# Performance work log

Hardware: AMD Instinct MI355X
Metric: run time of the kernel (lower is better)

## Reference

```python
import jax, jax.numpy as jnp
import numpy as np

KMAX, PH, PW, HID = 15, 16, 16, 64

def _rope(x):
    # x: (B, H, T, D); standard rotary, half-split rotation, base 10000
    D = x.shape[-1]; T = x.shape[-2]; half = D // 2
    inv_freq = 1.0 / (10000.0 ** (jnp.arange(half, dtype=jnp.float32) / half))
    ang = jnp.arange(T, dtype=jnp.float32)[:, None] * inv_freq[None, :]  # (T, half)
    cos, sin = jnp.cos(ang), jnp.sin(ang)
    x1, x2 = x[..., :half], x[..., half:]
    return jnp.concatenate([x1 * cos - x2 * sin, x1 * sin + x2 * cos], axis=-1)

def _normalize(v):
    return v / jnp.maximum(jnp.linalg.norm(v, axis=-1, keepdims=True), 1e-12)

def setup_inputs() -> dict:
    key = jax.random.key(0)
    ks = jax.random.split(key, 10)
    B, T, D = 2, 2048, 1024
    rel_in = KMAX + 2  # K gram cols + feat_a + delta
    s = D ** -0.5
    f32 = jnp.float32
    return {
        "x": jax.random.normal(ks[0], (B, T, D), f32),
        "Wi": jax.random.normal(ks[1], (D, D), f32) * s,
        "Wp": jax.random.normal(ks[2], (D, D), f32) * s,
        "palette": jax.random.normal(ks[3], (D, PH, PW), f32) * s,
        "W1": jax.random.normal(ks[4], (rel_in, HID), f32) * rel_in ** -0.5,
        "b1": jnp.zeros((HID,), f32),
        "W2": jax.random.normal(ks[5], (HID, HID), f32) * HID ** -0.5,
        "b2": jnp.zeros((HID,), f32),
        "Wc": jax.random.normal(ks[6], (HID, 2), f32) * HID ** -0.5,
        "bc": jnp.zeros((2,), f32),
        "Wm": jax.random.normal(ks[7], (HID, 1), f32) * HID ** -0.5,
        "bm": jnp.zeros((1,), f32),
        "Wo": jax.random.normal(ks[8], (1, D, D), f32) * s,
    }

def reference(x, Wi, Wp, palette, W1, b1, W2, b2, Wc, bc, Wm, bm, Wo):
    B, T, D = x.shape
    K = KMAX
    scale = D ** -0.5
    I = _rope((x @ Wi)[:, None])        # (B,1,T,D)
    P = _rope((x @ Wp)[:, None])[:, 0]  # (B,T,D)
    logits = jnp.einsum('bhtd,bsd->bhts', I, P) * scale
    causal = jnp.tril(jnp.ones((T, T), dtype=bool))
    logits = jnp.where(causal[None, None], logits, -jnp.inf)
    topk_val, topk_idx = jax.lax.top_k(logits, K)  # (B,1,T,K); T>=K so no pad branch
    keep = jnp.isfinite(topk_val)
    keep_f = keep.astype(x.dtype)
    # diagonal is always kept -> torch 'all_bad' fallback never fires
    P_sel = jax.vmap(lambda p, idx: p[idx])(P, topk_idx)      # (B,1,T,K,D)
    P_sel_norm = _normalize(P_sel) * keep_f[..., None]
    I_norm = _normalize(I)[:, :, :, None, :]                  # (B,1,T,1,D)
    feat_a = jnp.clip(jnp.sum(I_norm * P_sel_norm, -1), -1.0, 1.0) * keep_f
    G = jnp.clip(jnp.einsum('bhtkd,bhtjd->bhtkj', P_sel_norm, P_sel_norm), -1.0, 1.0)
    G = G * keep_f[..., :, None] * keep_f[..., None, :]
    t_range = jnp.arange(T)[None, None, :, None]
    delta = jnp.maximum((t_range - topk_idx).astype(x.dtype), 0.0) / float(max(1, T)) * keep_f
    rel = jnp.concatenate([G, feat_a[..., None], delta[..., None]], axis=-1)  # (B,1,T,K,K+2)
    h = jax.nn.gelu(rel @ W1 + b1, approximate=False)
    h = jax.nn.gelu(h @ W2 + b2, approximate=False)
    z = jnp.tanh(h @ Wc + bc)                                  # (B,1,T,K,2)
    mix = jnp.where(keep, (h @ Wm + bm)[..., 0], -jnp.inf)
    w = jnp.nan_to_num(jax.nn.softmax(mix, axis=-1))           # (B,1,T,K)
    # bilinear grid_sample: align_corners=True, padding_mode='border'
    gx, gy = z[:, 0, :, :, 0], z[:, 0, :, :, 1]                # (B,T,K)
    fx = jnp.clip((gx + 1.0) * 0.5 * (PW - 1), 0.0, PW - 1)
    fy = jnp.clip((gy + 1.0) * 0.5 * (PH - 1), 0.0, PH - 1)
    x0 = jnp.floor(fx).astype(jnp.int32); x1 = jnp.minimum(x0 + 1, PW - 1)
    y0 = jnp.floor(fy).astype(jnp.int32); y1 = jnp.minimum(y0 + 1, PH - 1)
    wx = fx - x0.astype(fx.dtype); wy = fy - y0.astype(fy.dtype)
    pal = palette.reshape(D, PH * PW)
    def g(yi, xi):  # -> (B,T,K,D)
        return jnp.moveaxis(pal[:, yi * PW + xi], 0, -1)
    samples = ((1 - wy) * (1 - wx))[..., None] * g(y0, x0) \
            + ((1 - wy) * wx)[..., None] * g(y0, x1) \
            + (wy * (1 - wx))[..., None] * g(y1, x0) \
            + (wy * wx)[..., None] * g(y1, x1)                 # (B,T,K,D)
    V = jnp.einsum('btkd,btk->btd', samples, w[:, 0])
    y = jnp.einsum('btd,dm->btm', V, Wo[0])  # einsum nrtd,rdm->nrtm then mean over r=1
    return y
```

## Files before the change

kernel.cpp:

```cpp
#include <hip/hip_runtime.h>
#include <math.h>

#define BATCH 2
#define T_LEN 2048
#define D_DIM 1024
#define KSEL  15
#define HIDN  64
#define NCAND 20

typedef short  bf16x8 __attribute__((ext_vector_type(8)));
typedef float  f32x4v __attribute__((ext_vector_type(4)));

__device__ __forceinline__ float geluf(float x) {
  return 0.5f * x * (1.0f + erff(x * 0.70710678118654752440f));
}

__device__ __forceinline__ unsigned short f32_to_bf16_rne(float x) {
  unsigned u = __builtin_bit_cast(unsigned, x);
  unsigned lsb = (u >> 16) & 1u;
  u += 0x7fffu + lsb;
  return (unsigned short)(u >> 16);
}
__device__ __forceinline__ float bf16_to_f32(unsigned short h) {
  unsigned u = ((unsigned)h) << 16;
  return __builtin_bit_cast(float, u);
}

__global__ void __launch_bounds__(256) xsplit3(const float* __restrict__ X,
                                               unsigned short* __restrict__ H,
                                               unsigned short* __restrict__ M,
                                               unsigned short* __restrict__ L)
{
  const size_t i = ((size_t)blockIdx.x * 256 + threadIdx.x) * 4;
  float4 v = *(const float4*)(X + i);
  ushort4 h, m, l;
  float r;
  h.x = f32_to_bf16_rne(v.x); r = v.x - bf16_to_f32(h.x);
  m.x = f32_to_bf16_rne(r);   l.x = f32_to_bf16_rne(r - bf16_to_f32(m.x));
  h.y = f32_to_bf16_rne(v.y); r = v.y - bf16_to_f32(h.y);
  m.y = f32_to_bf16_rne(r);   l.y = f32_to_bf16_rne(r - bf16_to_f32(m.y));
  h.z = f32_to_bf16_rne(v.z); r = v.z - bf16_to_f32(h.z);
  m.z = f32_to_bf16_rne(r);   l.z = f32_to_bf16_rne(r - bf16_to_f32(m.z));
  h.w = f32_to_bf16_rne(v.w); r = v.w - bf16_to_f32(h.w);
  m.w = f32_to_bf16_rne(r);   l.w = f32_to_bf16_rne(r - bf16_to_f32(m.w));
  *(ushort4*)(H + i) = h;
  *(ushort4*)(M + i) = m;
  *(ushort4*)(L + i) = l;
}

__global__ void __launch_bounds__(256) wsplit3T(const float* __restrict__ Wi,
                                                const float* __restrict__ Wp,
                                                unsigned short* __restrict__ WT)
{
  __shared__ float tile[64][65];
  const int k0 = blockIdx.y << 6, n0 = blockIdx.x << 6;
  const int z = blockIdx.z;
  const float* W = z ? Wp : Wi;
  unsigned short* H = WT + (size_t)z * 3 * 1024 * 1024;
  unsigned short* M = H + (size_t)1024 * 1024;
  unsigned short* L = M + (size_t)1024 * 1024;
  const int tid = threadIdx.x;
  for (int idx = tid; idx < 4096; idx += 256) {
    int r = idx >> 6, c = idx & 63;
    tile[r][c] = W[(size_t)(k0 + r) * D_DIM + n0 + c];
  }
  __syncthreads();
  for (int idx = tid; idx < 4096; idx += 256) {
    int n = idx >> 6, k = idx & 63;
    float v = tile[k][n];
    unsigned short h = f32_to_bf16_rne(v);
    float r1 = v - bf16_to_f32(h);
    unsigned short m = f32_to_bf16_rne(r1);
    unsigned short l = f32_to_bf16_rne(r1 - bf16_to_f32(m));
    size_t o = (size_t)(n0 + n) * D_DIM + k0 + k;
    H[o] = h; M[o] = m; L[o] = l;
  }
}

__global__ void __launch_bounds__(256) gemm3bf(
    const unsigned short* __restrict__ Xh, const unsigned short* __restrict__ Xm,
    const unsigned short* __restrict__ Xl, const unsigned short* __restrict__ WT,
    float* __restrict__ C)
{
  const int m0 = blockIdx.y << 6, n0 = blockIdx.x << 6;
  const int z = blockIdx.z;
  const unsigned short* BhT = WT + (size_t)z * 3 * 1024 * 1024;
  const unsigned short* BmT = BhT + (size_t)1024 * 1024;
  const unsigned short* BlT = BmT + (size_t)1024 * 1024;
  C += (size_t)z * 4096 * 1024;
  const int N = D_DIM, K = D_DIM;

  const int tid = threadIdx.x;
  const int w = tid >> 6, lane = tid & 63;
  const int kg = lane >> 4, lm = lane & 15;
  const int am0 = (w & 1) << 5;
  const int bn0 = (w >> 1) << 5;

  __shared__ unsigned short Ah[2][64][40], Am[2][64][40], Al[2][64][40];
  __shared__ unsigned short Bh[2][64][40], Bm[2][64][40], Bl[2][64][40];

  bf16x8 ones;
#pragma unroll
  for (int e = 0; e < 8; ++e) ones[e] = (short)0x3F80;

  for (int idx = tid; idx < 2048; idx += 256) {
    Ah[0][idx >> 5][idx & 31] = f32_to_bf16_rne((float)(idx >> 5));
    Bh[0][idx >> 5][idx & 31] = f32_to_bf16_rne((float)(idx >> 5));
  }
  __syncthreads();
  int mr[4], nc[4];
  {
    bf16x8 pa = *(const bf16x8*)&Ah[0][am0 + lm][kg << 3];
    bf16x8 pb = *(const bf16x8*)&Bh[0][bn0 + lm][kg << 3];
    f32x4v d1 = {0.f, 0.f, 0.f, 0.f}, d2 = {0.f, 0.f, 0.f, 0.f};
    d1 = __builtin_amdgcn_mfma_f32_16x16x32_bf16(pa, ones, d1, 0, 0, 0);
    d2 = __builtin_amdgcn_mfma_f32_16x16x32_bf16(ones, pb, d2, 0, 0, 0);
#pragma unroll
    for (int e = 0; e < 4; ++e) {
      mr[e] = ((int)d1[e]) >> 5;
      nc[e] = ((int)d2[e]) >> 5;
    }
  }
  __syncthreads();

  f32x4v ch[2][2], cm[2][2], cl[2][2];
#pragma unroll
  for (int i = 0; i < 2; ++i)
#pragma unroll
    for (int j = 0; j < 2; ++j) {
      ch[i][j] = (f32x4v){0.f, 0.f, 0.f, 0.f};
      cm[i][j] = (f32x4v){0.f, 0.f, 0.f, 0.f};
      cl[i][j] = (f32x4v){0.f, 0.f, 0.f, 0.f};
    }

  const int ar = tid >> 2, ak8 = (tid & 3) << 3;

  bf16x8 rah, ram, ral, rbh, rbm, rbl;

  {
    size_t ao = (size_t)(m0 + ar) * K + ak8;
    size_t bo = (size_t)(n0 + ar) * K + ak8;
    rah = *(const bf16x8*)(Xh + ao); ram = *(const bf16x8*)(Xm + ao);
    ral = *(const bf16x8*)(Xl + ao);
    rbh = *(const bf16x8*)(BhT + bo); rbm = *(const bf16x8*)(BmT + bo);
    rbl = *(const bf16x8*)(BlT + bo);
  }
  *(bf16x8*)&Ah[0][ar][ak8] = rah;
  *(bf16x8*)&Am[0][ar][ak8] = ram;
  *(bf16x8*)&Al[0][ar][ak8] = ral;
  *(bf16x8*)&Bh[0][ar][ak8] = rbh;
  *(bf16x8*)&Bm[0][ar][ak8] = rbm;
  *(bf16x8*)&Bl[0][ar][ak8] = rbl;
  __syncthreads();

  int buf = 0;
  for (int k0 = 0; k0 < K; k0 += 32) {
    const bool more = (k0 + 32) < K;
    if (more) {
      const int kn = k0 + 32;
      size_t ao = (size_t)(m0 + ar) * K + kn + ak8;
      size_t bo = (size_t)(n0 + ar) * K + kn + ak8;
      rah = *(const bf16x8*)(Xh + ao); ram = *(const bf16x8*)(Xm + ao);
      ral = *(const bf16x8*)(Xl + ao);
      rbh = *(const bf16x8*)(BhT + bo); rbm = *(const bf16x8*)(BmT + bo);
      rbl = *(const bf16x8*)(BlT + bo);
    }
    {
      bf16x8 a_h[2], a_m[2], a_l[2], b_h[2], b_m[2], b_l[2];
#pragma unroll
      for (int i = 0; i < 2; ++i) {
        const int rrow = am0 + (i << 4) + lm;
        a_h[i] = *(const bf16x8*)&Ah[buf][rrow][kg << 3];
        a_m[i] = *(const bf16x8*)&Am[buf][rrow][kg << 3];
        a_l[i] = *(const bf16x8*)&Al[buf][rrow][kg << 3];
        const int nrow = bn0 + (i << 4) + lm;
        b_h[i] = *(const bf16x8*)&Bh[buf][nrow][kg << 3];
        b_m[i] = *(const bf16x8*)&Bm[buf][nrow][kg << 3];
        b_l[i] = *(const bf16x8*)&Bl[buf][nrow][kg << 3];
      }
#pragma unroll
      for (int i = 0; i < 2; ++i)
#pragma unroll
        for (int j = 0; j < 2; ++j) {
          ch[i][j] = __builtin_amdgcn_mfma_f32_16x16x32_bf16(a_h[i], b_h[j], ch[i][j], 0, 0, 0);
          cm[i][j] = __builtin_amdgcn_mfma_f32_16x16x32_bf16(a_h[i], b_m[j], cm[i][j], 0, 0, 0);
          cm[i][j] = __builtin_amdgcn_mfma_f32_16x16x32_bf16(a_m[i], b_h[j], cm[i][j], 0, 0, 0);
          cl[i][j] = __builtin_amdgcn_mfma_f32_16x16x32_bf16(a_h[i], b_l[j], cl[i][j], 0, 0, 0);
          cl[i][j] = __builtin_amdgcn_mfma_f32_16x16x32_bf16(a_m[i], b_m[j], cl[i][j], 0, 0, 0);
          cl[i][j] = __builtin_amdgcn_mfma_f32_16x16x32_bf16(a_l[i], b_h[j], cl[i][j], 0, 0, 0);
        }
    }
    if (more) {
      const int nb = buf ^ 1;
      *(bf16x8*)&Ah[nb][ar][ak8] = rah;
      *(bf16x8*)&Am[nb][ar][ak8] = ram;
      *(bf16x8*)&Al[nb][ar][ak8] = ral;
      *(bf16x8*)&Bh[nb][ar][ak8] = rbh;
      *(bf16x8*)&Bm[nb][ar][ak8] = rbm;
      *(bf16x8*)&Bl[nb][ar][ak8] = rbl;
    }
    __syncthreads();
    buf ^= 1;
  }

#pragma unroll
  for (int i = 0; i < 2; ++i)
#pragma unroll
    for (int j = 0; j < 2; ++j)
#pragma unroll
      for (int e = 0; e < 4; ++e) {
        const int rrow = m0 + mr[e] + (i << 4);
        const int ccol = n0 + nc[e] + (j << 4);
        float v = (ch[i][j][e] + cm[i][j][e]) + cl[i][j][e];
        C[(size_t)rrow * N + ccol] = v;
      }
}

__global__ void __launch_bounds__(256) prep_kernel(float2* __restrict__ tab,
                                                   const float* __restrict__ pal,
                                                   float* __restrict__ palT)
{
  const int b = blockIdx.x;
  if (b < T_LEN) {
    const int t = b;
    for (int j = threadIdx.x; j < 512; j += 256) {
      double e = (double)j * (1.0 / 512.0);
      float pf = (float)pow(10000.0, e);
      float invf = 1.0f / pf;
      float angf = (float)t * invf;
      double s64, c64;
      sincos((double)angf, &s64, &c64);
      tab[(size_t)t * 512 + j] = make_float2((float)c64, (float)s64);
    }
  } else {
    const int bb = b - T_LEN;
    const int c = bb & 255, dg = bb >> 8;
    const int d = dg * 256 + threadIdx.x;
    palT[(size_t)c * D_DIM + d] = pal[(size_t)d * 256 + c];
  }
}

__global__ void __launch_bounds__(256) rope_norm_kernel(
    float* __restrict__ bI, float* __restrict__ bP,
    const float2* __restrict__ tab,
    float* __restrict__ nI, float* __restrict__ nP,
    unsigned short* __restrict__ Ih, unsigned short* __restrict__ Ph)
{
  const int row = blockIdx.x;
  const int t = row & (T_LEN - 1);
  const int tid = threadIdx.x;
  __shared__ double redI[4], redP[4];
  double ssI = 0.0, ssP = 0.0;
  const size_t off = (size_t)row * D_DIM;
  for (int j = tid; j < 512; j += 256) {
    float2 cs = tab[(size_t)t * 512 + j];
    float c = cs.x, s = cs.y;

    float a1 = bI[off + j], a2 = bI[off + 512 + j];
    float o1 = __fsub_rn(__fmul_rn(a1, c), __fmul_rn(a2, s));
    float o2 = __fadd_rn(__fmul_rn(a1, s), __fmul_rn(a2, c));
    bI[off + j] = o1; bI[off + 512 + j] = o2;
    Ih[off + j] = f32_to_bf16_rne(o1); Ih[off + 512 + j] = f32_to_bf16_rne(o2);
    ssI += (double)o1 * o1 + (double)o2 * o2;

    float p1 = bP[off + j], p2 = bP[off + 512 + j];
    float q1 = __fsub_rn(__fmul_rn(p1, c), __fmul_rn(p2, s));
    float q2 = __fadd_rn(__fmul_rn(p1, s), __fmul_rn(p2, c));
    bP[off + j] = q1; bP[off + 512 + j] = q2;
    Ph[off + j] = f32_to_bf16_rne(q1); Ph[off + 512 + j] = f32_to_bf16_rne(q2);
    ssP += (double)q1 * q1 + (double)q2 * q2;
  }
#pragma unroll
  for (int o = 32; o >= 1; o >>= 1) { ssI += __shfl_xor(ssI, o); ssP += __shfl_xor(ssP, o); }
  if ((tid & 63) == 0) { redI[tid >> 6] = ssI; redP[tid >> 6] = ssP; }
  __syncthreads();
  if (tid == 0) {
    nI[row] = fmaxf((float)sqrt(redI[0] + redI[1] + redI[2] + redI[3]), 1e-12f);
    nP[row] = fmaxf((float)sqrt(redP[0] + redP[1] + redP[2] + redP[3]), 1e-12f);
  }
}

__global__ void __launch_bounds__(256) screen_bf16(
    const unsigned short* __restrict__ Ih, const unsigned short* __restrict__ Ph,
    unsigned short* __restrict__ Ssc)
{
  int rem = blockIdx.x, bi = 0;
  while (rem >= (bi >> 1) + 1) { rem -= (bi >> 1) + 1; ++bi; }
  const int m0 = bi << 6, n0 = rem << 7;
  const int z = blockIdx.z;
  const unsigned short* A = Ih + (size_t)z * T_LEN * D_DIM;
  const unsigned short* B = Ph + (size_t)z * T_LEN * D_DIM;
  unsigned short* C = Ssc + (size_t)z * T_LEN * T_LEN;
  const int N = T_LEN, K = D_DIM;

  const int tid = threadIdx.x;
  const int w = tid >> 6, lane = tid & 63;
  const int kg = lane >> 4, lm = lane & 15;
  const int am0 = (w & 1) << 5;
  const int bn0 = (w >> 1) << 6;

  __shared__ unsigned short As_h[2][64][40];
  __shared__ unsigned short Bs_h[2][128][40];

  bf16x8 ones;
#pragma unroll
  for (int e = 0; e < 8; ++e) ones[e] = (short)0x3F80;

  for (int idx = tid; idx < 2048; idx += 256)
    As_h[0][idx >> 5][idx & 31] = f32_to_bf16_rne((float)(idx >> 5));
  for (int idx = tid; idx < 4096; idx += 256)
    Bs_h[0][idx >> 5][idx & 31] = f32_to_bf16_rne((float)(idx >> 5));
  __syncthreads();
  int mr[4], nc[4];
  {
    bf16x8 pa = *(const bf16x8*)&As_h[0][am0 + lm][kg << 3];
    bf16x8 pb = *(const bf16x8*)&Bs_h[0][bn0 + lm][kg << 3];
    f32x4v d1 = {0.f, 0.f, 0.f, 0.f}, d2 = {0.f, 0.f, 0.f, 0.f};
    d1 = __builtin_amdgcn_mfma_f32_16x16x32_bf16(pa, ones, d1, 0, 0, 0);
    d2 = __builtin_amdgcn_mfma_f32_16x16x32_bf16(ones, pb, d2, 0, 0, 0);
#pragma unroll
    for (int e = 0; e < 4; ++e) {
      mr[e] = ((int)d1[e]) >> 5;
      nc[e] = ((int)d2[e]) >> 5;
    }
  }
  __syncthreads();

  f32x4v c00 = {0,0,0,0}, c01 = {0,0,0,0}, c02 = {0,0,0,0}, c03 = {0,0,0,0};
  f32x4v c10 = {0,0,0,0}, c11 = {0,0,0,0}, c12 = {0,0,0,0}, c13 = {0,0,0,0};

  const int ar  = tid >> 2, ak8 = (tid & 3) << 3;
  const int bna = tid >> 2, bnb = 64 + (tid >> 2), bk8 = (tid & 3) << 3;

  bf16x8 ra, rb0, rb1;

  ra  = *(const bf16x8*)(A + (size_t)(m0 + ar) * K + ak8);
  rb0 = *(const bf16x8*)(B + (size_t)(n0 + bna) * K + bk8);
  rb1 = *(const bf16x8*)(B + (size_t)(n0 + bnb) * K + bk8);
  *(bf16x8*)&As_h[0][ar][ak8]  = ra;
  *(bf16x8*)&Bs_h[0][bna][bk8] = rb0;
  *(bf16x8*)&Bs_h[0][bnb][bk8] = rb1;
  __syncthreads();

  int buf = 0;
  for (int k0 = 0; k0 < K; k0 += 32) {
    const bool more = (k0 + 32) < K;
    if (more) {
      const int kn = k0 + 32;
      ra  = *(const bf16x8*)(A + (size_t)(m0 + ar) * K + kn + ak8);
      rb0 = *(const bf16x8*)(B + (size_t)(n0 + bna) * K + kn + bk8);
      rb1 = *(const bf16x8*)(B + (size_t)(n0 + bnb) * K + kn + bk8);
    }
    {
      bf16x8 a0 = *(const bf16x8*)&As_h[buf][am0 + lm][kg << 3];
      bf16x8 a1 = *(const bf16x8*)&As_h[buf][am0 + 16 + lm][kg << 3];
      bf16x8 b0 = *(const bf16x8*)&Bs_h[buf][bn0 + lm][kg << 3];
      bf16x8 b1 = *(const bf16x8*)&Bs_h[buf][bn0 + 16 + lm][kg << 3];
      bf16x8 b2 = *(const bf16x8*)&Bs_h[buf][bn0 + 32 + lm][kg << 3];
      bf16x8 b3 = *(const bf16x8*)&Bs_h[buf][bn0 + 48 + lm][kg << 3];
      c00 = __builtin_amdgcn_mfma_f32_16x16x32_bf16(a0, b0, c00, 0, 0, 0);
      c01 = __builtin_amdgcn_mfma_f32_16x16x32_bf16(a0, b1, c01, 0, 0, 0);
      c02 = __builtin_amdgcn_mfma_f32_16x16x32_bf16(a0, b2, c02, 0, 0, 0);
      c03 = __builtin_amdgcn_mfma_f32_16x16x32_bf16(a0, b3, c03, 0, 0, 0);
      c10 = __builtin_amdgcn_mfma_f32_16x16x32_bf16(a1, b0, c10, 0, 0, 0);
      c11 = __builtin_amdgcn_mfma_f32_16x16x32_bf16(a1, b1, c11, 0, 0, 0);
      c12 = __builtin_amdgcn_mfma_f32_16x16x32_bf16(a1, b2, c12, 0, 0, 0);
      c13 = __builtin_amdgcn_mfma_f32_16x16x32_bf16(a1, b3, c13, 0, 0, 0);
    }
    if (more) {
      const int nb = buf ^ 1;
      *(bf16x8*)&As_h[nb][ar][ak8]  = ra;
      *(bf16x8*)&Bs_h[nb][bna][bk8] = rb0;
      *(bf16x8*)&Bs_h[nb][bnb][bk8] = rb1;
    }
    __syncthreads();
    buf ^= 1;
  }

#pragma unroll
  for (int e = 0; e < 4; ++e) {
    const size_t r0 = (size_t)(m0 + mr[e]) * N;
    const size_t r1 = r0 + (size_t)16 * N;
    const int c = n0 + nc[e];
    C[r0 + c +  0] = f32_to_bf16_rne(c00[e]);
    C[r0 + c + 16] = f32_to_bf16_rne(c01[e]);
    C[r0 + c + 32] = f32_to_bf16_rne(c02[e]);
    C[r0 + c + 48] = f32_to_bf16_rne(c03[e]);
    C[r1 + c +  0] = f32_to_bf16_rne(c10[e]);
    C[r1 + c + 16] = f32_to_bf16_rne(c11[e]);
    C[r1 + c + 32] = f32_to_bf16_rne(c12[e]);
    C[r1 + c + 48] = f32_to_bf16_rne(c13[e]);
  }
}

__global__ void __launch_bounds__(256) topk_screen(const unsigned short* __restrict__ Ssc,
                                                   int* __restrict__ cand)
{
  const int b = blockIdx.y;
  const unsigned short* S = Ssc + (size_t)b * T_LEN * T_LEN;
  const int wave = threadIdx.x >> 6, lane = threadIdx.x & 63;
  const int t = blockIdx.x * 4 + wave;
  const unsigned short* rowp = S + (size_t)t * T_LEN;
  float v[32];
#pragma unroll
  for (int i = 0; i < 32; ++i) {
    int s = lane + (i << 6);
    v[i] = (s <= t) ? bf16_to_f32(rowp[s]) : -INFINITY;
  }
  float pv = INFINITY; int pidx = -1;
  int* outp = cand + ((size_t)b * T_LEN + t) * NCAND;
  for (int k = 0; k < NCAND; ++k) {
    float bv = -INFINITY; int bi = 0x7fffffff;
#pragma unroll
    for (int i = 0; i < 32; ++i) {
      int s = lane + (i << 6);
      float vv = v[i];
      bool elig = (vv < pv) || (vv == pv && s > pidx);
      if (elig && vv > bv) { bv = vv; bi = s; }
    }
#pragma unroll
    for (int o = 32; o >= 1; o >>= 1) {
      float ov = __shfl_xor(bv, o);
      int oi = __shfl_xor(bi, o);
      if (ov > bv || (ov == bv && oi < bi)) { bv = ov; bi = oi; }
    }
    pv = bv; pidx = bi;
    if (lane == 0) outp[k] = (bi == 0x7fffffff || bv == -INFINITY) ? -1 : bi;
  }
}

__global__ void __launch_bounds__(256) rescore_kernel(
    const float* __restrict__ I, const float* __restrict__ P,
    const int* __restrict__ cand, int* __restrict__ idx)
{
  const int row = blockIdx.x;
  const int base = row & ~(T_LEN - 1);
  const int tid = threadIdx.x;
  const int w = tid >> 6, lane = tid & 63;

  __shared__ float valS[NCAND];
  __shared__ int   sidxS[NCAND];
  __shared__ int   candS[NCAND];

  if (tid < NCAND) candS[tid] = cand[(size_t)row * NCAND + tid];
  __syncthreads();

  double iv[16];
  const float* irow = I + (size_t)row * D_DIM;
#pragma unroll
  for (int j = 0; j < 16; ++j) iv[j] = (double)irow[lane + (j << 6)];

  for (int c = w; c < NCAND; c += 4) {
    int s = candS[c];
    double acc = 0.0;
    if (s >= 0) {
      const float* prow = P + ((size_t)base + s) * D_DIM;
#pragma unroll
      for (int j = 0; j < 16; ++j)
        acc = fma(iv[j], (double)prow[lane + (j << 6)], acc);
    }
#pragma unroll
    for (int o = 32; o >= 1; o >>= 1) acc += __shfl_xor(acc, o);
    if (lane == 0) {
      valS[c] = (s >= 0) ? (float)(acc * 0.03125) : -INFINITY;
      sidxS[c] = s;
    }
  }
  __syncthreads();
  if (tid == 0) {
    bool taken[NCAND];
#pragma unroll
    for (int c = 0; c < NCAND; ++c) taken[c] = false;
    int* outp = idx + (size_t)row * 16;
    for (int k = 0; k < KSEL; ++k) {
      float best = -INFINITY; int bidx = 0x7fffffff; int bc = -1;
      for (int c = 0; c < NCAND; ++c) {
        if (taken[c] || sidxS[c] < 0) continue;
        float v = valS[c];
        if (v > best || (v == best && sidxS[c] < bidx)) { best = v; bidx = sidxS[c]; bc = c; }
      }
      if (bc >= 0) { taken[bc] = true; outp[k] = bidx; }
      else outp[k] = 0;
    }
  }
}

__global__ void __launch_bounds__(256) woconvT(const float* __restrict__ Wo,
                                               unsigned short* __restrict__ HT,
                                               unsigned short* __restrict__ LT)
{
  __shared__ float tile[64][65];
  const int k0 = blockIdx.y << 6, n0 = blockIdx.x << 6;
  const int tid = threadIdx.x;
  for (int idx = tid; idx < 4096; idx += 256) {
    int r = idx >> 6, c = idx & 63;
    tile[r][c] = Wo[(size_t)(k0 + r) * D_DIM + n0 + c];
  }
  __syncthreads();
  for (int idx = tid; idx < 4096; idx += 256) {
    int n = idx >> 6, k = idx & 63;
    float v = tile[k][n];
    unsigned short h = f32_to_bf16_rne(v);
    HT[(size_t)(n0 + n) * D_DIM + k0 + k] = h;
    LT[(size_t)(n0 + n) * D_DIM + k0 + k] = f32_to_bf16_rne(v - bf16_to_f32(h));
  }
}

__global__ void __launch_bounds__(256) relmlp_kernel(
    const unsigned short* __restrict__ Ih, const unsigned short* __restrict__ Ph,
    const float* __restrict__ nI, const float* __restrict__ nP,
    const int* __restrict__ topk,
    const float* __restrict__ W1, const float* __restrict__ b1,
    const float* __restrict__ W2, const float* __restrict__ b2,
    const float* __restrict__ Wc, const float* __restrict__ bc,
    const float* __restrict__ Wm, const float* __restrict__ bm,
    const float* __restrict__ palT,
    unsigned short* __restrict__ Vh, unsigned short* __restrict__ Vl)
{
  const int row = blockIdx.x;
  const int t = row & (T_LEN - 1);
  const int base = row & ~(T_LEN - 1);
  const int nk = (t + 1 < KSEL) ? (t + 1) : KSEL;
  const int tid = threadIdx.x;
  const int lane = tid & 63;

  __shared__ unsigned short vecU[16][1032];
  __shared__ unsigned short pb[16][36];
  __shared__ float gS[16][16];
  __shared__ float relS[KSEL][17];
  __shared__ float h1S[KSEL][HIDN];
  __shared__ float h2S[KSEL][HIDN];
  __shared__ float nrmS[16];
  __shared__ int   sidxS[16];
  __shared__ float mixS[KSEL], wS[KSEL], zxS[KSEL], zyS[KSEL];
  __shared__ float coefS[4 * KSEL];
  __shared__ int   cellS[4 * KSEL];

  if (tid < 16) {
    int s = t;
    if (tid >= 1) s = (tid <= nk) ? topk[(size_t)row * 16 + (tid - 1)] : 0;
    sidxS[tid] = s;
    nrmS[tid] = (tid == 0) ? nI[row] : nP[base + s];
  }
  if (tid < 64) {
#pragma unroll
    for (int i = 0; i < 8; ++i) {
      int e = (tid << 3) + i;
      pb[e >> 5][e & 31] = f32_to_bf16_rne((float)(e >> 5));
    }
  }
  __syncthreads();

#pragma unroll
  for (int i = 0; i < 8; ++i) {
    int c = (tid << 3) + i;
    int rr = c >> 7;
    int off = (c & 127) << 3;
    bf16x8 v = {0, 0, 0, 0, 0, 0, 0, 0};
    if (rr <= nk) {
      const unsigned short* src = (rr == 0)
          ? (Ih + (size_t)row * D_DIM)
          : (Ph + ((size_t)base + sidxS[rr]) * D_DIM);
      v = *(const bf16x8*)(src + off);
    }
    *(bf16x8*)&vecU[rr][off] = v;
  }
  __syncthreads();

  if (tid < 64) {
    const int lm = lane & 15, kg = lane >> 4;
    bf16x8 ones;
#pragma unroll
    for (int e = 0; e < 8; ++e) ones[e] = (short)0x3F80;
    bf16x8 pa = *(const bf16x8*)&pb[lm][kg << 3];
    f32x4v d1 = {0.f, 0.f, 0.f, 0.f}, d2 = {0.f, 0.f, 0.f, 0.f};
    d1 = __builtin_amdgcn_mfma_f32_16x16x32_bf16(pa, ones, d1, 0, 0, 0);
    d2 = __builtin_amdgcn_mfma_f32_16x16x32_bf16(ones, pa, d2, 0, 0, 0);
    int mr[4], nc[4];
#pragma unroll
    for (int e = 0; e < 4; ++e) {
      mr[e] = ((int)d1[e]) >> 5;
      nc[e] = ((int)d2[e]) >> 5;
    }
    f32x4v acc = {0.f, 0.f, 0.f, 0.f};
#pragma unroll
    for (int ks = 0; ks < 32; ++ks) {
      bf16x8 a = *(const bf16x8*)&vecU[lm][(ks << 5) + (kg << 3)];
      acc = __builtin_amdgcn_mfma_f32_16x16x32_bf16(a, a, acc, 0, 0, 0);
    }
#pragma unroll
    for (int e = 0; e < 4; ++e) {
      int pi2 = mr[e], pj2 = nc[e];
      float g = 0.f;
      if (pi2 <= nk && pj2 <= nk) {
        g = acc[e] / (nrmS[pi2] * nrmS[pj2]);
        g = fminf(fmaxf(g, -1.f), 1.f);
      }
      gS[pi2][pj2] = g;
    }
  }
  __syncthreads();

  if (tid < KSEL * 17) {
    int k = tid / 17, f = tid % 17;
    float v = 0.f;
    if (k < nk) {
      if (f < KSEL)        v = (f < nk) ? gS[k + 1][f + 1] : 0.f;
      else if (f == KSEL)  v = gS[0][k + 1];
      else                 v = (float)(t - sidxS[k + 1]) * (1.0f / (float)T_LEN);
    }
    relS[k][f] = v;
  }
  __syncthreads();

  for (int o = tid; o < KSEL * HIDN; o += 256) {
    int k = o >> 6, m = o & 63;
    float a = b1[m];
#pragma unroll
    for (int f = 0; f < 17; ++f) a = fmaf(relS[k][f], W1[f * HIDN + m], a);
    h1S[k][m] = geluf(a);
  }
  __syncthreads();
  for (int o = tid; o < KSEL * HIDN; o += 256) {
    int k = o >> 6, m = o & 63;
    float a = b2[m];
#pragma unroll 8
    for (int n = 0; n < HIDN; ++n) a = fmaf(h1S[k][n], W2[n * HIDN + m], a);
    h2S[k][m] = geluf(a);
  }
  __syncthreads();
  if (tid < KSEL) {
    float a0 = 0.f, a1 = 0.f, am = 0.f;
#pragma unroll 8
    for (int n = 0; n < HIDN; ++n) {
      float h = h2S[tid][n];
      a0 = fmaf(h, Wc[n * 2 + 0], a0);
      a1 = fmaf(h, Wc[n * 2 + 1], a1);
      am = fmaf(h, Wm[n], am);
    }
    zxS[tid] = tanhf(a0 + bc[0]);
    zyS[tid] = tanhf(a1 + bc[1]);
    mixS[tid] = am + bm[0];
  }
  __syncthreads();
  if (tid == 0) {
    float mx = -INFINITY;
    for (int k = 0; k < nk; ++k) mx = fmaxf(mx, mixS[k]);
    float ssum = 0.f;
    for (int k = 0; k < nk; ++k) { float e = expf(mixS[k] - mx); wS[k] = e; ssum += e; }
    float inv = 1.f / ssum;
    for (int k = 0; k < nk; ++k) wS[k] *= inv;
  }
  __syncthreads();
  if (tid < KSEL) {
    int k = tid;
    if (k < nk) {
      float w = wS[k];
      float fx = fminf(fmaxf((zxS[k] + 1.f) * 0.5f * 15.f, 0.f), 15.f);
      float fy = fminf(fmaxf((zyS[k] + 1.f) * 0.5f * 15.f, 0.f), 15.f);
      int x0 = (int)floorf(fx); int x1i = (x0 + 1 < 15) ? x0 + 1 : 15;
      int y0 = (int)floorf(fy); int y1i = (y0 + 1 < 15) ? y0 + 1 : 15;
      float wx = fx - (float)x0, wy = fy - (float)y0;
      cellS[k * 4 + 0] = y0 * 16 + x0;   coefS[k * 4 + 0] = w * (1.f - wy) * (1.f - wx);
      cellS[k * 4 + 1] = y0 * 16 + x1i;  coefS[k * 4 + 1] = w * (1.f - wy) * wx;
      cellS[k * 4 + 2] = y1i * 16 + x0;  coefS[k * 4 + 2] = w * wy * (1.f - wx);
      cellS[k * 4 + 3] = y1i * 16 + x1i; coefS[k * 4 + 3] = w * wy * wx;
    } else {
      cellS[k * 4 + 0] = cellS[k * 4 + 1] = cellS[k * 4 + 2] = cellS[k * 4 + 3] = 0;
      coefS[k * 4 + 0] = coefS[k * 4 + 1] = coefS[k * 4 + 2] = coefS[k * 4 + 3] = 0.f;
    }
  }
  __syncthreads();
  const int nj = 4 * nk;
  for (int d = tid; d < D_DIM; d += 256) {
    float a = 0.f;
    for (int j = 0; j < nj; ++j)
      a = fmaf(coefS[j], palT[(size_t)cellS[j] * D_DIM + d], a);
    unsigned short h = f32_to_bf16_rne(a);
    Vh[(size_t)row * D_DIM + d] = h;
    Vl[(size_t)row * D_DIM + d] = f32_to_bf16_rne(a - bf16_to_f32(h));
  }
}

__global__ void __launch_bounds__(256) gemmbf(
    const unsigned short* __restrict__ Ah, const unsigned short* __restrict__ Al,
    const unsigned short* __restrict__ BhT, const unsigned short* __restrict__ BlT,
    float* __restrict__ C, int N, int K)
{
  const int m0 = blockIdx.y << 6, n0 = blockIdx.x << 7;
  const int tid = threadIdx.x;
  const int w = tid >> 6, lane = tid & 63;
  const int kg = lane >> 4, lm = lane & 15;
  const int am0 = (w & 1) << 5;
  const int bn0 = (w >> 1) << 6;

  __shared__ unsigned short As_h[2][64][40],  As_l[2][64][40];
  __shared__ unsigned short Bs_h[2][128][40], Bs_l[2][128][40];

  bf16x8 ones;
#pragma unroll
  for (int e = 0; e < 8; ++e) ones[e] = (short)0x3F80;

  for (int idx = tid; idx < 2048; idx += 256)
    As_h[0][idx >> 5][idx & 31] = f32_to_bf16_rne((float)(idx >> 5));
  for (int idx = tid; idx < 4096; idx += 256)
    Bs_h[0][idx >> 5][idx & 31] = f32_to_bf16_rne((float)(idx >> 5));
  __syncthreads();
  int mr[4], nc[4];
  {
    bf16x8 pa = *(const bf16x8*)&As_h[0][am0 + lm][kg << 3];
    bf16x8 pb = *(const bf16x8*)&Bs_h[0][bn0 + lm][kg << 3];
    f32x4v d1 = {0.f, 0.f, 0.f, 0.f}, d2 = {0.f, 0.f, 0.f, 0.f};
    d1 = __builtin_amdgcn_mfma_f32_16x16x32_bf16(pa, ones, d1, 0, 0, 0);
    d2 = __builtin_amdgcn_mfma_f32_16x16x32_bf16(ones, pb, d2, 0, 0, 0);
#pragma unroll
    for (int e = 0; e < 4; ++e) {
      mr[e] = ((int)d1[e]) >> 5;
      nc[e] = ((int)d2[e]) >> 5;
    }
  }
  __syncthreads();

  f32x4v c00 = {0,0,0,0}, c01 = {0,0,0,0}, c02 = {0,0,0,0}, c03 = {0,0,0,0};
  f32x4v c10 = {0,0,0,0}, c11 = {0,0,0,0}, c12 = {0,0,0,0}, c13 = {0,0,0,0};

  const int ar  = tid >> 2, ak8 = (tid & 3) << 3;
  const int bna = tid >> 2, bnb = 64 + (tid >> 2), bk8 = (tid & 3) << 3;

  bf16x8 rah, ral, rbh0, rbl0, rbh1, rbl1;

  rah  = *(const bf16x8*)(Ah  + (size_t)(m0 + ar) * K + ak8);
  ral  = *(const bf16x8*)(Al  + (size_t)(m0 + ar) * K + ak8);
  rbh0 = *(const bf16x8*)(BhT + (size_t)(n0 + bna) * K + bk8);
  rbl0 = *(const bf16x8*)(BlT + (size_t)(n0 + bna) * K + bk8);
  rbh1 = *(const bf16x8*)(BhT + (size_t)(n0 + bnb) * K + bk8);
  rbl1 = *(const bf16x8*)(BlT + (size_t)(n0 + bnb) * K + bk8);
  *(bf16x8*)&As_h[0][ar][ak8]  = rah;
  *(bf16x8*)&As_l[0][ar][ak8]  = ral;
  *(bf16x8*)&Bs_h[0][bna][bk8] = rbh0;
  *(bf16x8*)&Bs_l[0][bna][bk8] = rbl0;
  *(bf16x8*)&Bs_h[0][bnb][bk8] = rbh1;
  *(bf16x8*)&Bs_l[0][bnb][bk8] = rbl1;
  __syncthreads();

  int buf = 0;
  for (int k0 = 0; k0 < K; k0 += 32) {
    const bool more = (k0 + 32) < K;
    if (more) {
      const int kn = k0 + 32;
      rah  = *(const bf16x8*)(Ah  + (size_t)(m0 + ar) * K + kn + ak8);
      ral  = *(const bf16x8*)(Al  + (size_t)(m0 + ar) * K + kn + ak8);
      rbh0 = *(const bf16x8*)(BhT + (size_t)(n0 + bna) * K + kn + bk8);
      rbl0 = *(const bf16x8*)(BlT + (size_t)(n0 + bna) * K + kn + bk8);
      rbh1 = *(const bf16x8*)(BhT + (size_t)(n0 + bnb) * K + kn + bk8);
      rbl1 = *(const bf16x8*)(BlT + (size_t)(n0 + bnb) * K + kn + bk8);
    }
    {
      bf16x8 ah0 = *(const bf16x8*)&As_h[buf][am0 + lm][kg << 3];
      bf16x8 ah1 = *(const bf16x8*)&As_h[buf][am0 + 16 + lm][kg << 3];
      bf16x8 al0 = *(const bf16x8*)&As_l[buf][am0 + lm][kg << 3];
      bf16x8 al1 = *(const bf16x8*)&As_l[buf][am0 + 16 + lm][kg << 3];
      bf16x8 bh0 = *(const bf16x8*)&Bs_h[buf][bn0 + lm][kg << 3];
      bf16x8 bh1 = *(const bf16x8*)&Bs_h[buf][bn0 + 16 + lm][kg << 3];
      bf16x8 bh2 = *(const bf16x8*)&Bs_h[buf][bn0 + 32 + lm][kg << 3];
      bf16x8 bh3 = *(const bf16x8*)&Bs_h[buf][bn0 + 48 + lm][kg << 3];
      bf16x8 bl0 = *(const bf16x8*)&Bs_l[buf][bn0 + lm][kg << 3];
      bf16x8 bl1 = *(const bf16x8*)&Bs_l[buf][bn0 + 16 + lm][kg << 3];
      bf16x8 bl2 = *(const bf16x8*)&Bs_l[buf][bn0 + 32 + lm][kg << 3];
      bf16x8 bl3 = *(const bf16x8*)&Bs_l[buf][bn0 + 48 + lm][kg << 3];

      c00 = __builtin_amdgcn_mfma_f32_16x16x32_bf16(ah0, bh0, c00, 0, 0, 0);
      c01 = __builtin_amdgcn_mfma_f32_16x16x32_bf16(ah0, bh1, c01, 0, 0, 0);
      c02 = __builtin_amdgcn_mfma_f32_16x16x32_bf16(ah0, bh2, c02, 0, 0, 0);
      c03 = __builtin_amdgcn_mfma_f32_16x16x32_bf16(ah0, bh3, c03, 0, 0, 0);
      c10 = __builtin_amdgcn_mfma_f32_16x16x32_bf16(ah1, bh0, c10, 0, 0, 0);
      c11 = __builtin_amdgcn_mfma_f32_16x16x32_bf16(ah1, bh1, c11, 0, 0, 0);
      c12 = __builtin_amdgcn_mfma_f32_16x16x32_bf16(ah1, bh2, c12, 0, 0, 0);
      c13 = __builtin_amdgcn_mfma_f32_16x16x32_bf16(ah1, bh3, c13, 0, 0, 0);

      c00 = __builtin_amdgcn_mfma_f32_16x16x32_bf16(ah0, bl0, c00, 0, 0, 0);
      c01 = __builtin_amdgcn_mfma_f32_16x16x32_bf16(ah0, bl1, c01, 0, 0, 0);
      c02 = __builtin_amdgcn_mfma_f32_16x16x32_bf16(ah0, bl2, c02, 0, 0, 0);
      c03 = __builtin_amdgcn_mfma_f32_16x16x32_bf16(ah0, bl3, c03, 0, 0, 0);
      c10 = __builtin_amdgcn_mfma_f32_16x16x32_bf16(ah1, bl0, c10, 0, 0, 0);
      c11 = __builtin_amdgcn_mfma_f32_16x16x32_bf16(ah1, bl1, c11, 0, 0, 0);
      c12 = __builtin_amdgcn_mfma_f32_16x16x32_bf16(ah1, bl2, c12, 0, 0, 0);
      c13 = __builtin_amdgcn_mfma_f32_16x16x32_bf16(ah1, bl3, c13, 0, 0, 0);

      c00 = __builtin_amdgcn_mfma_f32_16x16x32_bf16(al0, bh0, c00, 0, 0, 0);
      c01 = __builtin_amdgcn_mfma_f32_16x16x32_bf16(al0, bh1, c01, 0, 0, 0);
      c02 = __builtin_amdgcn_mfma_f32_16x16x32_bf16(al0, bh2, c02, 0, 0, 0);
      c03 = __builtin_amdgcn_mfma_f32_16x16x32_bf16(al0, bh3, c03, 0, 0, 0);
      c10 = __builtin_amdgcn_mfma_f32_16x16x32_bf16(al1, bh0, c10, 0, 0, 0);
      c11 = __builtin_amdgcn_mfma_f32_16x16x32_bf16(al1, bh1, c11, 0, 0, 0);
      c12 = __builtin_amdgcn_mfma_f32_16x16x32_bf16(al1, bh2, c12, 0, 0, 0);
      c13 = __builtin_amdgcn_mfma_f32_16x16x32_bf16(al1, bh3, c13, 0, 0, 0);
    }
    if (more) {
      const int nb = buf ^ 1;
      *(bf16x8*)&As_h[nb][ar][ak8]  = rah;
      *(bf16x8*)&As_l[nb][ar][ak8]  = ral;
      *(bf16x8*)&Bs_h[nb][bna][bk8] = rbh0;
      *(bf16x8*)&Bs_l[nb][bna][bk8] = rbl0;
      *(bf16x8*)&Bs_h[nb][bnb][bk8] = rbh1;
      *(bf16x8*)&Bs_l[nb][bnb][bk8] = rbl1;
    }
    __syncthreads();
    buf ^= 1;
  }

#pragma unroll
  for (int e = 0; e < 4; ++e) {
    const size_t r0 = (size_t)(m0 + mr[e]) * N;
    const size_t r1 = r0 + (size_t)16 * N;
    const int c = n0 + nc[e];
    C[r0 + c +  0] = c00[e];
    C[r0 + c + 16] = c01[e];
    C[r0 + c + 32] = c02[e];
    C[r0 + c + 48] = c03[e];
    C[r1 + c +  0] = c10[e];
    C[r1 + c + 16] = c11[e];
    C[r1 + c + 32] = c12[e];
    C[r1 + c + 48] = c13[e];
  }
}

extern "C" void kernel_launch(void* const* d_in, const int* in_sizes, int n_in,
                              void* d_out, int out_size, void* d_ws, size_t ws_size,
                              hipStream_t stream)
{
  (void)in_sizes; (void)n_in; (void)out_size; (void)ws_size;
  const float* x   = (const float*)d_in[0];
  const float* Wi  = (const float*)d_in[1];
  const float* Wp  = (const float*)d_in[2];
  const float* pal = (const float*)d_in[3];
  const float* W1  = (const float*)d_in[4];
  const float* b1  = (const float*)d_in[5];
  const float* W2  = (const float*)d_in[6];
  const float* b2  = (const float*)d_in[7];
  const float* Wc  = (const float*)d_in[8];
  const float* bc  = (const float*)d_in[9];
  const float* Wm  = (const float*)d_in[10];
  const float* bm  = (const float*)d_in[11];
  const float* Wo  = (const float*)d_in[12];
  float* out = (float*)d_out;

  float* w = (float*)d_ws;
  float* palT = w;  w += (size_t)256 * D_DIM;
  float* I    = w;  w += (size_t)BATCH * T_LEN * D_DIM;
  float* P    = w;  w += (size_t)BATCH * T_LEN * D_DIM;
  float* Sb   = w;  w += (size_t)BATCH * T_LEN * T_LEN;
  float* nIb  = w;  w += (size_t)BATCH * T_LEN;
  float* nPb  = w;  w += (size_t)BATCH * T_LEN;
  int*   idx  = (int*)w;  w += (size_t)BATCH * T_LEN * 16;
  int*   cand = (int*)w;

  unsigned short* Xh = (unsigned short*)Sb;
  unsigned short* Xm = Xh + (size_t)4096 * 1024;
  unsigned short* Xl = Xm + (size_t)4096 * 1024;
  unsigned short* WT = (unsigned short*)d_out;

  float2* tab = (float2*)Sb;
  unsigned short* Ssc = (unsigned short*)Sb;
  unsigned short* Ih  = (unsigned short*)(Sb + (size_t)4 * 1024 * 1024);
  unsigned short* Ph  = Ih + (size_t)4 * 1024 * 1024;
  unsigned short* Vh  = (unsigned short*)Sb;
  unsigned short* Vl  = Vh + (size_t)4 * 1024 * 1024;
  unsigned short* WohT = (unsigned short*)P;
  unsigned short* WolT = WohT + (size_t)D_DIM * D_DIM;

  const int MROWS = BATCH * T_LEN;

  xsplit3<<<(MROWS * D_DIM) / (256 * 4), 256, 0, stream>>>(x, Xh, Xm, Xl);
  wsplit3T<<<dim3(D_DIM / 64, D_DIM / 64, 2), 256, 0, stream>>>(Wi, Wp, WT);

  gemm3bf<<<dim3(D_DIM / 64, MROWS / 64, 2), 256, 0, stream>>>(
      Xh, Xm, Xl, WT, I);

  prep_kernel<<<T_LEN + 1024, 256, 0, stream>>>(tab, pal, palT);

  rope_norm_kernel<<<MROWS, 256, 0, stream>>>(I, P, tab, nIb, nPb, Ih, Ph);

  screen_bf16<<<dim3(272, 1, 2), 256, 0, stream>>>(Ih, Ph, Ssc);

  topk_screen<<<dim3(T_LEN / 4, BATCH), 256, 0, stream>>>(Ssc, cand);

  rescore_kernel<<<MROWS, 256, 0, stream>>>(I, P, cand, idx);

  woconvT<<<dim3(D_DIM / 64, D_DIM / 64), 256, 0, stream>>>(Wo, WohT, WolT);

  relmlp_kernel<<<MROWS, 256, 0, stream>>>(Ih, Ph, nIb, nPb, idx,
                                           W1, b1, W2, b2, Wc, bc, Wm, bm,
                                           palT, Vh, Vl);

  gemmbf<<<dim3(D_DIM / 128, MROWS / 64), 256, 0, stream>>>(
      Vh, Vl, WohT, WolT, out, D_DIM, D_DIM);
}
```

Measured before the change: 536.6 us.

## Process one row per wavefront in relation-MLP kernel, loading Gram operands directly

Restructures relmlp_kernel so each 256-thread block handles four rows, one per wavefront, instead of one row per block. It drops the 33 KB shared-memory staging of the selected vectors: the Gram MFMA now reads its bf16 operands straight from global memory. The MLP layers are mapped so each lane owns one hidden unit, which removes the mostly idle threads of the old layout. This reduces per-row block overhead and shared-memory footprint, so occupancy should rise, at the cost of more serial work per wave and redundant global loads of the A operand.

```diff
diff --git a/kernel.cpp b/kernel.cpp
--- a/kernel.cpp
+++ b/kernel.cpp
@@ -517,165 +517,148 @@
     const float* __restrict__ palT,
     unsigned short* __restrict__ Vh, unsigned short* __restrict__ Vl)
 {
-  const int row = blockIdx.x;
-  const int t = row & (T_LEN - 1);
+  const int wv   = threadIdx.x >> 6;
+  const int lane = threadIdx.x & 63;
+  const int row  = (blockIdx.x << 2) + wv;
+  const int t    = row & (T_LEN - 1);
   const int base = row & ~(T_LEN - 1);
-  const int nk = (t + 1 < KSEL) ? (t + 1) : KSEL;
-  const int tid = threadIdx.x;
-  const int lane = tid & 63;
-
-  __shared__ unsigned short vecU[16][1032];
-  __shared__ unsigned short pb[16][36];
-  __shared__ float gS[16][16];
-  __shared__ float relS[KSEL][17];
-  __shared__ float h1S[KSEL][HIDN];
-  __shared__ float h2S[KSEL][HIDN];
-  __shared__ float nrmS[16];
-  __shared__ int   sidxS[16];
-  __shared__ float mixS[KSEL], wS[KSEL], zxS[KSEL], zyS[KSEL];
-  __shared__ float coefS[4 * KSEL];
-  __shared__ int   cellS[4 * KSEL];
-
-  if (tid < 16) {
+  const int nk   = (t + 1 < KSEL) ? (t + 1) : KSEL;
+
+  __shared__ int   sidxS[4][16];
+  __shared__ float nrmS[4][16];
+  __shared__ float gS[4][16][16];
+  __shared__ float relS[4][KSEL][18];
+  __shared__ float h1S[4][KSEL][HIDN];
+  __shared__ float h2S[4][KSEL][HIDN];
+  __shared__ float mixS[4][KSEL], wSS[4][KSEL], zxS[4][KSEL], zyS[4][KSEL];
+  __shared__ float coefS[4][4 * KSEL];
+  __shared__ int   cellS[4][4 * KSEL];
+
+  if (lane < 16) {
     int s = t;
-    if (tid >= 1) s = (tid <= nk) ? topk[(size_t)row * 16 + (tid - 1)] : 0;
-    sidxS[tid] = s;
-    nrmS[tid] = (tid == 0) ? nI[row] : nP[base + s];
-  }
-  if (tid < 64) {
-#pragma unroll
-    for (int i = 0; i < 8; ++i) {
-      int e = (tid << 3) + i;
-      pb[e >> 5][e & 31] = f32_to_bf16_rne((float)(e >> 5));
-    }
-  }
-  __syncthreads();
-
-#pragma unroll
-  for (int i = 0; i < 8; ++i) {
-    int c = (tid << 3) + i;
-    int rr = c >> 7;
-    int off = (c & 127) << 3;
-    bf16x8 v = {0, 0, 0, 0, 0, 0, 0, 0};
-    if (rr <= nk) {
-      const unsigned short* src = (rr == 0)
-          ? (Ih + (size_t)row * D_DIM)
-          : (Ph + ((size_t)base + sidxS[rr]) * D_DIM);
-      v = *(const bf16x8*)(src + off);
-    }
-    *(bf16x8*)&vecU[rr][off] = v;
-  }
-  __syncthreads();
-
-  if (tid < 64) {
-    const int lm = lane & 15, kg = lane >> 4;
-    bf16x8 ones;
-#pragma unroll
-    for (int e = 0; e < 8; ++e) ones[e] = (short)0x3F80;
-    bf16x8 pa = *(const bf16x8*)&pb[lm][kg << 3];
+    if (lane >= 1) s = (lane <= nk) ? topk[(size_t)row * 16 + (lane - 1)] : 0;
+    sidxS[wv][lane] = s;
+    nrmS[wv][lane] = (lane == 0) ? nI[row] : nP[base + s];
+  }
+  __syncthreads();
+
+  const int lm = lane & 15, kg = lane >> 4;
+  {
+    const unsigned short* src = (lm == 0)
+        ? (Ih + (size_t)row * D_DIM)
+        : (Ph + ((size_t)base + sidxS[wv][lm]) * D_DIM);
+    f32x4v acc = {0.f, 0.f, 0.f, 0.f};
+#pragma unroll
+    for (int ks = 0; ks < 32; ++ks) {
+      bf16x8 a;
+      if (lm <= nk) a = *(const bf16x8*)(src + (ks << 5) + (kg << 3));
+      else {
+        bf16x8 zz = {0, 0, 0, 0, 0, 0, 0, 0};
+        a = zz;
+      }
+      acc = __builtin_amdgcn_mfma_f32_16x16x32_bf16(a, a, acc, 0, 0, 0);
+    }
+    bf16x8 pa, ones;
+    unsigned short lmb = f32_to_bf16_rne((float)lm);
+#pragma unroll
+    for (int e = 0; e < 8; ++e) { pa[e] = (short)lmb; ones[e] = (short)0x3F80; }
     f32x4v d1 = {0.f, 0.f, 0.f, 0.f}, d2 = {0.f, 0.f, 0.f, 0.f};
     d1 = __builtin_amdgcn_mfma_f32_16x16x32_bf16(pa, ones, d1, 0, 0, 0);
     d2 = __builtin_amdgcn_mfma_f32_16x16x32_bf16(ones, pa, d2, 0, 0, 0);
-    int mr[4], nc[4];
 #pragma unroll
     for (int e = 0; e < 4; ++e) {
-      mr[e] = ((int)d1[e]) >> 5;
-      nc[e] = ((int)d2[e]) >> 5;
-    }
-    f32x4v acc = {0.f, 0.f, 0.f, 0.f};
-#pragma unroll
-    for (int ks = 0; ks < 32; ++ks) {
-      bf16x8 a = *(const bf16x8*)&vecU[lm][(ks << 5) + (kg << 3)];
-      acc = __builtin_amdgcn_mfma_f32_16x16x32_bf16(a, a, acc, 0, 0, 0);
-    }
-#pragma unroll
-    for (int e = 0; e < 4; ++e) {
-      int pi2 = mr[e], pj2 = nc[e];
+      int pi2 = ((int)d1[e]) >> 5;
+      int pj2 = ((int)d2[e]) >> 5;
       float g = 0.f;
       if (pi2 <= nk && pj2 <= nk) {
-        g = acc[e] / (nrmS[pi2] * nrmS[pj2]);
+        g = acc[e] / (nrmS[wv][pi2] * nrmS[wv][pj2]);
         g = fminf(fmaxf(g, -1.f), 1.f);
       }
-      gS[pi2][pj2] = g;
-    }
-  }
-  __syncthreads();
-
-  if (tid < KSEL * 17) {
-    int k = tid / 17, f = tid % 17;
+      gS[wv][pi2][pj2] = g;
+    }
+  }
+  __syncthreads();
+
+  for (int o = lane; o < KSEL * 17; o += 64) {
+    int k = o / 17, f = o % 17;
     float v = 0.f;
     if (k < nk) {
-      if (f < KSEL)        v = (f < nk) ? gS[k + 1][f + 1] : 0.f;
-      else if (f == KSEL)  v = gS[0][k + 1];
-      else                 v = (float)(t - sidxS[k + 1]) * (1.0f / (float)T_LEN);
-    }
-    relS[k][f] = v;
-  }
-  __syncthreads();
-
-  for (int o = tid; o < KSEL * HIDN; o += 256) {
-    int k = o >> 6, m = o & 63;
-    float a = b1[m];
-#pragma unroll
-    for (int f = 0; f < 17; ++f) a = fmaf(relS[k][f], W1[f * HIDN + m], a);
-    h1S[k][m] = geluf(a);
-  }
-  __syncthreads();
-  for (int o = tid; o < KSEL * HIDN; o += 256) {
-    int k = o >> 6, m = o & 63;
-    float a = b2[m];
+      if (f < KSEL)        v = (f < nk) ? gS[wv][k + 1][f + 1] : 0.f;
+      else if (f == KSEL)  v = gS[wv][0][k + 1];
+      else                 v = (float)(t - sidxS[wv][k + 1]) * (1.0f / (float)T_LEN);
+    }
+    relS[wv][k][f] = v;
+  }
+  __syncthreads();
+
+#pragma unroll
+  for (int k = 0; k < KSEL; ++k) {
+    float a = b1[lane];
+#pragma unroll
+    for (int f = 0; f < 17; ++f) a = fmaf(relS[wv][k][f], W1[f * HIDN + lane], a);
+    h1S[wv][k][lane] = geluf(a);
+  }
+  __syncthreads();
+
+#pragma unroll
+  for (int k = 0; k < KSEL; ++k) {
+    float a = b2[lane];
 #pragma unroll 8
-    for (int n = 0; n < HIDN; ++n) a = fmaf(h1S[k][n], W2[n * HIDN + m], a);
-    h2S[k][m] = geluf(a);
-  }
-  __syncthreads();
-  if (tid < KSEL) {
+    for (int n = 0; n < HIDN; ++n) a = fmaf(h1S[wv][k][n], W2[n * HIDN + lane], a);
+    h2S[wv][k][lane] = geluf(a);
+  }
+  __syncthreads();
+
+  if (lane < KSEL) {
     float a0 = 0.f, a1 = 0.f, am = 0.f;
 #pragma unroll 8
     for (int n = 0; n < HIDN; ++n) {
-      float h = h2S[tid][n];
+      float h = h2S[wv][lane][n];
       a0 = fmaf(h, Wc[n * 2 + 0], a0);
       a1 = fmaf(h, Wc[n * 2 + 1], a1);
       am = fmaf(h, Wm[n], am);
     }
-    zxS[tid] = tanhf(a0 + bc[0]);
-    zyS[tid] = tanhf(a1 + bc[1]);
-    mixS[tid] = am + bm[0];
-  }
-  __syncthreads();
-  if (tid == 0) {
+    zxS[wv][lane] = tanhf(a0 + bc[0]);
+    zyS[wv][lane] = tanhf(a1 + bc[1]);
+    mixS[wv][lane] = am + bm[0];
+  }
+  __syncthreads();
+
+  if (lane == 0) {
     float mx = -INFINITY;
-    for (int k = 0; k < nk; ++k) mx = fmaxf(mx, mixS[k]);
+    for (int k = 0; k < nk; ++k) mx = fmaxf(mx, mixS[wv][k]);
     float ssum = 0.f;
-    for (int k = 0; k < nk; ++k) { float e = expf(mixS[k] - mx); wS[k] = e; ssum += e; }
+    for (int k = 0; k < nk; ++k) { float e = expf(mixS[wv][k] - mx); wSS[wv][k] = e; ssum += e; }
     float inv = 1.f / ssum;
-    for (int k = 0; k < nk; ++k) wS[k] *= inv;
-  }
-  __syncthreads();
-  if (tid < KSEL) {
-    int k = tid;
+    for (int k = 0; k < nk; ++k) wSS[wv][k] *= inv;
+  }
+  __syncthreads();
+
+  if (lane < KSEL) {
+    int k = lane;
     if (k < nk) {
-      float w = wS[k];
-      float fx = fminf(fmaxf((zxS[k] + 1.f) * 0.5f * 15.f, 0.f), 15.f);
-      float fy = fminf(fmaxf((zyS[k] + 1.f) * 0.5f * 15.f, 0.f), 15.f);
+      float w = wSS[wv][k];
+      float fx = fminf(fmaxf((zxS[wv][k] + 1.f) * 0.5f * 15.f, 0.f), 15.f);
+      float fy = fminf(fmaxf((zyS[wv][k] + 1.f) * 0.5f * 15.f, 0.f), 15.f);
       int x0 = (int)floorf(fx); int x1i = (x0 + 1 < 15) ? x0 + 1 : 15;
       int y0 = (int)floorf(fy); int y1i = (y0 + 1 < 15) ? y0 + 1 : 15;
       float wx = fx - (float)x0, wy = fy - (float)y0;
-      cellS[k * 4 + 0] = y0 * 16 + x0;   coefS[k * 4 + 0] = w * (1.f - wy) * (1.f - wx);
-      cellS[k * 4 + 1] = y0 * 16 + x1i;  coefS[k * 4 + 1] = w * (1.f - wy) * wx;
-      cellS[k * 4 + 2] = y1i * 16 + x0;  coefS[k * 4 + 2] = w * wy * (1.f - wx);
-      cellS[k * 4 + 3] = y1i * 16 + x1i; coefS[k * 4 + 3] = w * wy * wx;
+      cellS[wv][k * 4 + 0] = y0 * 16 + x0;   coefS[wv][k * 4 + 0] = w * (1.f - wy) * (1.f - wx);
+      cellS[wv][k * 4 + 1] = y0 * 16 + x1i;  coefS[wv][k * 4 + 1] = w * (1.f - wy) * wx;
+      cellS[wv][k * 4 + 2] = y1i * 16 + x0;  coefS[wv][k * 4 + 2] = w * wy * (1.f - wx);
+      cellS[wv][k * 4 + 3] = y1i * 16 + x1i; coefS[wv][k * 4 + 3] = w * wy * wx;
     } else {
-      cellS[k * 4 + 0] = cellS[k * 4 + 1] = cellS[k * 4 + 2] = cellS[k * 4 + 3] = 0;
-      coefS[k * 4 + 0] = coefS[k * 4 + 1] = coefS[k * 4 + 2] = coefS[k * 4 + 3] = 0.f;
-    }
-  }
-  __syncthreads();
+      cellS[wv][k * 4 + 0] = cellS[wv][k * 4 + 1] = cellS[wv][k * 4 + 2] = cellS[wv][k * 4 + 3] = 0;
+      coefS[wv][k * 4 + 0] = coefS[wv][k * 4 + 1] = coefS[wv][k * 4 + 2] = coefS[wv][k * 4 + 3] = 0.f;
+    }
+  }
+  __syncthreads();
+
   const int nj = 4 * nk;
-  for (int d = tid; d < D_DIM; d += 256) {
+  for (int d = lane; d < D_DIM; d += 64) {
     float a = 0.f;
     for (int j = 0; j < nj; ++j)
-      a = fmaf(coefS[j], palT[(size_t)cellS[j] * D_DIM + d], a);
+      a = fmaf(coefS[wv][j], palT[(size_t)cellS[wv][j] * D_DIM + d], a);
     unsigned short h = f32_to_bf16_rne(a);
     Vh[(size_t)row * D_DIM + d] = h;
     Vl[(size_t)row * D_DIM + d] = f32_to_bf16_rne(a - bf16_to_f32(h));
@@ -889,9 +872,9 @@
 
   woconvT<<<dim3(D_DIM / 64, D_DIM / 64), 256, 0, stream>>>(Wo, WohT, WolT);
 
-  relmlp_kernel<<<MROWS, 256, 0, stream>>>(Ih, Ph, nIb, nPb, idx,
-                                           W1, b1, W2, b2, Wc, bc, Wm, bm,
-                                           palT, Vh, Vl);
+  relmlp_kernel<<<MROWS / 4, 256, 0, stream>>>(Ih, Ph, nIb, nPb, idx,
+                                               W1, b1, W2, b2, Wc, bc, Wm, bm,
+                                               palT, Vh, Vl);
 
   gemmbf<<<dim3(D_DIM / 128, MROWS / 64), 256, 0, stream>>>(
       Vh, Vl, WohT, WolT, out, D_DIM, D_DIM);
```

Result: no change. 532.7 us (-0.7%).
